# Performance work log

Hardware: AMD Instinct MI355X
Metric: run time of the kernel (lower is better)

The kernel has to match this reference:

```python
import jax, jax.numpy as jnp
import numpy as np
from math import sqrt

LOCAL_WINDOW = 32
STRIDE = 64


def _sparse_mask(L):
    # L_Q == L_K path of DozerAttention:
    #  - local window: diagonals at offsets 0..local_window//2 (both signs)
    #  - strided: diagonals at offsets 0, stride+1, 2*(stride+1), ... (both signs)
    i = jnp.arange(L)[:, None]
    j = jnp.arange(L)[None, :]
    d = jnp.abs(i - j)
    local = d <= (LOCAL_WINDOW // 2)
    strided = (d % (STRIDE + 1)) == 0
    return (local | strided).astype(jnp.float32)  # [L, L]


def setup_inputs() -> dict:
    key = jax.random.key(0)
    B, L, H, D = 2, 2048, 8, 64
    kq, kk, kv = jax.random.split(key, 3)
    queries = jax.random.normal(kq, (B, L, H, D), dtype=jnp.float32)
    keys = jax.random.normal(kk, (B, L, H, D), dtype=jnp.float32)
    values = jax.random.normal(kv, (B, L, H, D), dtype=jnp.float32)
    # TriangularCausalMask: True above the diagonal -> masked with -inf
    causal = jnp.triu(jnp.ones((L, L), dtype=bool), k=1)
    attn_mask = jnp.broadcast_to(causal[None, None], (B, 1, L, L))
    return {"queries": queries, "keys": keys, "values": values, "attn_mask": attn_mask}


def reference(queries, keys, values, attn_mask):
    B, L, H, D = queries.shape
    scale = 1.0 / sqrt(D)
    sm = _sparse_mask(L)  # [L, L]
    # Original fills a zero-initialized dense score tensor only at selected key
    # columns per query row; equivalent to dense QK^T elementwise-masked by sm
    # (non-selected entries stay exactly 0, NOT -inf -- faithful quirk).
    scores = jnp.einsum('blhe,bshe->bhls', queries, keys) * sm  # [B,H,L,L]
    scores = jnp.where(attn_mask, -jnp.inf, scores)
    A = jax.nn.softmax(scale * scores, axis=-1)  # dropout p=0.0 in this config
    V = jnp.einsum('bhls,bshd->blhd', A, values)  # [B,L,H,D]
    return V
```

## Files before the change

### kernel.cpp

```cpp
#include <hip/hip_runtime.h>
#include <hip/hip_bf16.h>

#define B_ 2
#define L_ 2048
#define H_ 8
#define D_ 64
#define SP_ 65
#define NC_ 128
#define RS_ 512

typedef __attribute__((ext_vector_type(8))) short bf16x8;
typedef __attribute__((ext_vector_type(16))) float f32x16;

static __device__ inline short f2bf(float x) {
    return __builtin_bit_cast(short, __float2bfloat16(x));
}

static __device__ inline bf16x8 ld8_bf16(const float* __restrict__ p) {
    float4 a = *(const float4*)p;
    float4 b = *(const float4*)(p + 4);
    bf16x8 r;
    r[0]=f2bf(a.x); r[1]=f2bf(a.y); r[2]=f2bf(a.z); r[3]=f2bf(a.w);
    r[4]=f2bf(b.x); r[5]=f2bf(b.y); r[6]=f2bf(b.z); r[7]=f2bf(b.w);
    return r;
}

static __device__ inline bf16x8 ones_frag() {
    bf16x8 r;
    short o = f2bf(1.f);
    #pragma unroll
    for (int t = 0; t < 8; ++t) r[t] = o;
    return r;
}

__global__ __launch_bounds__(256) void partials_k(const float* __restrict__ q,
                                                  const float* __restrict__ kk,
                                                  const float* __restrict__ v,
                                                  float* __restrict__ csum1,
                                                  float* __restrict__ pA,
                                                  float* __restrict__ zA,
                                                  float* __restrict__ pB,
                                                  float* __restrict__ zB) {
    __shared__ float LDS[4608];
    int wib  = threadIdx.x >> 6;
    int lane = threadIdx.x & 63;
    int half = lane >> 5, ln = lane & 31;
    int blk  = blockIdx.x;

    if (blk < 512) {
        int tb = wib >> 1;
        int hf = wib & 1;
        int team = blk * 2 + tb;
        int bh = team >> 6;
        int T  = (team & 63) << 5;
        int h = bh & 7, b = bh >> 3;
        const size_t base = (size_t)b * L_ * RS_ + (size_t)h * D_;
        float* Pw = LDS + tb * 2176;
        int d0 = 32 * hf;

        bf16x8 bv[4];
        #pragma unroll
        for (int kb = 0; kb < 4; ++kb) {
            #pragma unroll
            for (int jj = 0; jj < 8; ++jj) {
                int jr = T - 16 + kb * 16 + half * 8 + jj;
                jr = jr < 0 ? 0 : (jr > L_ - 1 ? L_ - 1 : jr);
                bv[kb][jj] = f2bf(v[base + (size_t)jr * RS_ + d0 + ln]);
            }
        }

        const float* qrow = q + base + (size_t)(T + ln) * RS_;
        bf16x8 aq[4];
        #pragma unroll
        for (int kb = 0; kb < 4; ++kb) aq[kb] = ld8_bf16(qrow + kb * 16 + half * 8);

        int j = T - 16 + 32 * hf + ln;
        j = j < 0 ? 0 : (j > L_ - 1 ? L_ - 1 : j);
        const float* krow = kk + base + (size_t)j * RS_;
        f32x16 acc = {};
        #pragma unroll
        for (int kb = 0; kb < 4; ++kb) {
            bf16x8 kf = ld8_bf16(krow + kb * 16 + half * 8);
            acc = __builtin_amdgcn_mfma_f32_32x32x16_bf16(aq[kb], kf, acc, 0, 0, 0);
        }

        #pragma unroll
        for (int r = 0; r < 16; ++r) {
            int m = (r & 3) + 8 * (r >> 2) + 4 * half;
            float w;
            if (hf == 0) {
                bool act = (ln >= m) && (ln <= m + 16) && (T - 16 + ln >= 0);
                w = act ? (__expf(0.125f * acc[r]) - 1.f) : 0.f;
                if ((m < 16) && (ln >= 16) && (ln <= m + 16)) w += 1.f;
            } else {
                bool act = (ln <= m - 16);
                w = act ? (__expf(0.125f * acc[r]) - 1.f) : 0.f;
                if ((m >= 16) && (ln <= m - 16)) w += 1.f;
            }
            Pw[m * 68 + d0 + ln] = w;
        }
        __syncthreads();

        f32x16 p = {}; f32x16 po = {};
        bf16x8 ones = ones_frag();
        #pragma unroll
        for (int kb = 0; kb < 4; ++kb) {
            int k0 = kb * 16 + half * 8;
            const float* pr = &Pw[ln * 68 + k0];
            float4 x = *(const float4*)pr;
            float4 y = *(const float4*)(pr + 4);
            bf16x8 ap;
            ap[0]=f2bf(x.x); ap[1]=f2bf(x.y); ap[2]=f2bf(x.z); ap[3]=f2bf(x.w);
            ap[4]=f2bf(y.x); ap[5]=f2bf(y.y); ap[6]=f2bf(y.z); ap[7]=f2bf(y.w);
            p = __builtin_amdgcn_mfma_f32_32x32x16_bf16(ap, bv[kb], p, 0, 0, 0);
            if (hf == 0)
                po = __builtin_amdgcn_mfma_f32_32x32x16_bf16(ap, ones, po, 0, 0, 0);
        }

        float* pAr = pA + (size_t)bh * L_ * D_;
        float* zAr = zA + (size_t)bh * L_;
        #pragma unroll
        for (int r = 0; r < 16; ++r) {
            int m = (r & 3) + 8 * (r >> 2) + 4 * half;
            int i = T + m;
            pAr[(size_t)i * D_ + d0 + ln] = p[r];
            if (hf == 0 && ln == 0)
                zAr[i] = po[r] - (float)((m & 15) + 1);
        }
    } else if (blk < 772) {
        int us = (blk - 512) * 4 + wib;
        int bh = us / SP_;
        int r  = us % SP_;
        int h = bh & 7, b = bh >> 3;
        const size_t base = (size_t)b * L_ * RS_ + (size_t)h * D_;
        float* Pw = LDS + wib * 1152;

        bf16x8 bv0[2], bv1[2];
        #pragma unroll
        for (int kb = 0; kb < 2; ++kb) {
            int k0 = kb * 16 + half * 8;
            #pragma unroll
            for (int jj = 0; jj < 8; ++jj) {
                int lv = r + SP_ * (k0 + jj);
                lv = lv > L_ - 1 ? L_ - 1 : lv;
                const float* vr = v + base + (size_t)lv * RS_;
                bv0[kb][jj] = f2bf(vr[ln]);
                bv1[kb][jj] = f2bf(vr[32 + ln]);
            }
        }

        int lq = r + SP_ * ln;
        int lqc = lq > L_ - 1 ? L_ - 1 : lq;
        const float* qrow = q  + base + (size_t)lqc * RS_;
        const float* krow = kk + base + (size_t)lqc * RS_;
        f32x16 acc = {};
        #pragma unroll
        for (int kb = 0; kb < 4; ++kb) {
            bf16x8 a  = ld8_bf16(qrow + kb * 16 + half * 8);
            bf16x8 bb = ld8_bf16(krow + kb * 16 + half * 8);
            acc = __builtin_amdgcn_mfma_f32_32x32x16_bf16(a, bb, acc, 0, 0, 0);
        }
        #pragma unroll
        for (int rg = 0; rg < 16; ++rg) {
            int m = (rg & 3) + 8 * (rg >> 2) + 4 * half;
            bool act = (ln < m) && (r + SP_ * m < L_);
            Pw[m * 36 + ln] = act ? (__expf(0.125f * acc[rg]) - 1.f) : 0.f;
        }
        __syncthreads();

        f32x16 p0 = {}; f32x16 p1 = {}; f32x16 po = {};
        bf16x8 ones = ones_frag();
        #pragma unroll
        for (int kb = 0; kb < 2; ++kb) {
            int k0 = kb * 16 + half * 8;
            const float* pr = &Pw[ln * 36 + k0];
            float4 x = *(const float4*)pr;
            float4 y = *(const float4*)(pr + 4);
            bf16x8 ap;
            ap[0]=f2bf(x.x); ap[1]=f2bf(x.y); ap[2]=f2bf(x.z); ap[3]=f2bf(x.w);
            ap[4]=f2bf(y.x); ap[5]=f2bf(y.y); ap[6]=f2bf(y.z); ap[7]=f2bf(y.w);
            p0 = __builtin_amdgcn_mfma_f32_32x32x16_bf16(ap, bv0[kb], p0, 0, 0, 0);
            p1 = __builtin_amdgcn_mfma_f32_32x32x16_bf16(ap, bv1[kb], p1, 0, 0, 0);
            po = __builtin_amdgcn_mfma_f32_32x32x16_bf16(ap, ones,    po, 0, 0, 0);
        }
        float* pBr = pB + (size_t)bh * L_ * D_;
        float* zBr = zB + (size_t)bh * L_;
        #pragma unroll
        for (int rg = 0; rg < 16; ++rg) {
            int m = (rg & 3) + 8 * (rg >> 2) + 4 * half;
            int l = r + SP_ * m;
            if (l < L_) {
                pBr[(size_t)l * D_ + ln]      = p0[rg];
                pBr[(size_t)l * D_ + 32 + ln] = p1[rg];
                if (ln == 0) zBr[l] = po[rg];
            }
        }
    } else {
        int uc = (blk - 772) * 4 + wib;
        int c = uc & (NC_ - 1);
        int bh = uc >> 7;
        int h = bh & 7, b = bh >> 3;
        const float* vb = v + (size_t)(b * L_ + c * 16) * RS_ + h * D_ + lane;
        float s = 0.f;
        #pragma unroll
        for (int l = 0; l < 16; ++l) s += vb[l * RS_];
        csum1[(size_t)uc * D_ + lane] = s;
    }
}

__global__ __launch_bounds__(256) void combine_k(const float* __restrict__ csum1,
                                                 const float* __restrict__ pA,
                                                 const float* __restrict__ zA,
                                                 const float* __restrict__ pB,
                                                 const float* __restrict__ zB,
                                                 float* __restrict__ out) {
    int wib  = threadIdx.x >> 6;
    int lane = threadIdx.x & 63;
    int u = blockIdx.x * 4 + wib;
    int bh = u >> 8;
    int g  = u & 255;
    int i0 = g << 3;
    int c1 = i0 >> 4;
    int h = bh & 7, b = bh >> 3;

    const float* cs1 = csum1 + (size_t)bh * NC_ * D_ + lane;
    float s0 = 0.f, s1 = 0.f, s2 = 0.f, s3 = 0.f;
    int cc = 0;
    for (; cc + 4 <= c1; cc += 4) {
        s0 += cs1[(cc + 0) * D_]; s1 += cs1[(cc + 1) * D_];
        s2 += cs1[(cc + 2) * D_]; s3 += cs1[(cc + 3) * D_];
    }
    for (; cc < c1; ++cc) s0 += cs1[cc * D_];
    float pr = (s0 + s1) + (s2 + s3);

    const float* pAr = pA + (size_t)bh * L_ * D_;
    const float* pBr = pB + (size_t)bh * L_ * D_;
    const float* zAr = zA + (size_t)bh * L_;
    const float* zBr = zB + (size_t)bh * L_;
    const size_t obase = (size_t)b * L_ * RS_ + (size_t)h * D_;

    #pragma unroll
    for (int r = 0; r < 8; ++r) {
        int i = i0 + r;
        float num = pAr[(size_t)i * D_ + lane] + pBr[(size_t)i * D_ + lane] + pr;
        float inv = 1.f / (zAr[i] + zBr[i] + (float)(i + 1));
        out[obase + (size_t)i * RS_ + lane] = num * inv;
    }
}

extern "C" void kernel_launch(void* const* d_in, const int* in_sizes, int n_in,
                              void* d_out, int out_size, void* d_ws, size_t ws_size,
                              hipStream_t stream) {
    const float* q = (const float*)d_in[0];
    const float* k = (const float*)d_in[1];
    const float* v = (const float*)d_in[2];
    float* out = (float*)d_out;

    float* csum1 = (float*)d_ws;
    float* pA    = csum1 + (size_t)B_ * H_ * NC_ * D_;
    float* zA    = pA    + (size_t)B_ * H_ * L_ * D_;
    float* pB    = zA    + (size_t)B_ * H_ * L_;
    float* zB    = pB    + (size_t)B_ * H_ * L_ * D_;

    partials_k<<<1284, 256, 0, stream>>>(q, k, v, csum1, pA, zA, pB, zB);
    combine_k<<<1024, 256, 0, stream>>>(csum1, pA, zA, pB, zB, out);
}
```

Baseline: 112.0 us.

## Fuse local-window attention into the combine kernel to drop pA/zA round trip

Moves the local-window QK/softmax-weight/PV computation out of the partials kernel and into the final combine kernel, so its partial numerator and normalizer stay in registers and LDS instead of being written to and reread from global workspace. The first kernel now handles only the strided partials and the chunk column sums. This removes the pA/zA global traffic and the separate combine pass. In exchange, the second kernel becomes heavier with fewer blocks, and the two phases rebalance across the launches.

```diff
diff --git a/kernel.cpp b/kernel.cpp
--- a/kernel.cpp
+++ b/kernel.cpp
@@ -33,102 +33,20 @@
     return r;
 }
 
-__global__ __launch_bounds__(256) void partials_k(const float* __restrict__ q,
-                                                  const float* __restrict__ kk,
-                                                  const float* __restrict__ v,
-                                                  float* __restrict__ csum1,
-                                                  float* __restrict__ pA,
-                                                  float* __restrict__ zA,
-                                                  float* __restrict__ pB,
-                                                  float* __restrict__ zB) {
+__global__ __launch_bounds__(256) void stride_csum_k(const float* __restrict__ q,
+                                                     const float* __restrict__ kk,
+                                                     const float* __restrict__ v,
+                                                     float* __restrict__ csum1,
+                                                     float* __restrict__ pB,
+                                                     float* __restrict__ zB) {
     __shared__ float LDS[4608];
     int wib  = threadIdx.x >> 6;
     int lane = threadIdx.x & 63;
     int half = lane >> 5, ln = lane & 31;
     int blk  = blockIdx.x;
 
-    if (blk < 512) {
-        int tb = wib >> 1;
-        int hf = wib & 1;
-        int team = blk * 2 + tb;
-        int bh = team >> 6;
-        int T  = (team & 63) << 5;
-        int h = bh & 7, b = bh >> 3;
-        const size_t base = (size_t)b * L_ * RS_ + (size_t)h * D_;
-        float* Pw = LDS + tb * 2176;
-        int d0 = 32 * hf;
-
-        bf16x8 bv[4];
-        #pragma unroll
-        for (int kb = 0; kb < 4; ++kb) {
-            #pragma unroll
-            for (int jj = 0; jj < 8; ++jj) {
-                int jr = T - 16 + kb * 16 + half * 8 + jj;
-                jr = jr < 0 ? 0 : (jr > L_ - 1 ? L_ - 1 : jr);
-                bv[kb][jj] = f2bf(v[base + (size_t)jr * RS_ + d0 + ln]);
-            }
-        }
-
-        const float* qrow = q + base + (size_t)(T + ln) * RS_;
-        bf16x8 aq[4];
-        #pragma unroll
-        for (int kb = 0; kb < 4; ++kb) aq[kb] = ld8_bf16(qrow + kb * 16 + half * 8);
-
-        int j = T - 16 + 32 * hf + ln;
-        j = j < 0 ? 0 : (j > L_ - 1 ? L_ - 1 : j);
-        const float* krow = kk + base + (size_t)j * RS_;
-        f32x16 acc = {};
-        #pragma unroll
-        for (int kb = 0; kb < 4; ++kb) {
-            bf16x8 kf = ld8_bf16(krow + kb * 16 + half * 8);
-            acc = __builtin_amdgcn_mfma_f32_32x32x16_bf16(aq[kb], kf, acc, 0, 0, 0);
-        }
-
-        #pragma unroll
-        for (int r = 0; r < 16; ++r) {
-            int m = (r & 3) + 8 * (r >> 2) + 4 * half;
-            float w;
-            if (hf == 0) {
-                bool act = (ln >= m) && (ln <= m + 16) && (T - 16 + ln >= 0);
-                w = act ? (__expf(0.125f * acc[r]) - 1.f) : 0.f;
-                if ((m < 16) && (ln >= 16) && (ln <= m + 16)) w += 1.f;
-            } else {
-                bool act = (ln <= m - 16);
-                w = act ? (__expf(0.125f * acc[r]) - 1.f) : 0.f;
-                if ((m >= 16) && (ln <= m - 16)) w += 1.f;
-            }
-            Pw[m * 68 + d0 + ln] = w;
-        }
-        __syncthreads();
-
-        f32x16 p = {}; f32x16 po = {};
-        bf16x8 ones = ones_frag();
-        #pragma unroll
-        for (int kb = 0; kb < 4; ++kb) {
-            int k0 = kb * 16 + half * 8;
-            const float* pr = &Pw[ln * 68 + k0];
-            float4 x = *(const float4*)pr;
-            float4 y = *(const float4*)(pr + 4);
-            bf16x8 ap;
-            ap[0]=f2bf(x.x); ap[1]=f2bf(x.y); ap[2]=f2bf(x.z); ap[3]=f2bf(x.w);
-            ap[4]=f2bf(y.x); ap[5]=f2bf(y.y); ap[6]=f2bf(y.z); ap[7]=f2bf(y.w);
-            p = __builtin_amdgcn_mfma_f32_32x32x16_bf16(ap, bv[kb], p, 0, 0, 0);
-            if (hf == 0)
-                po = __builtin_amdgcn_mfma_f32_32x32x16_bf16(ap, ones, po, 0, 0, 0);
-        }
-
-        float* pAr = pA + (size_t)bh * L_ * D_;
-        float* zAr = zA + (size_t)bh * L_;
-        #pragma unroll
-        for (int r = 0; r < 16; ++r) {
-            int m = (r & 3) + 8 * (r >> 2) + 4 * half;
-            int i = T + m;
-            pAr[(size_t)i * D_ + d0 + ln] = p[r];
-            if (hf == 0 && ln == 0)
-                zAr[i] = po[r] - (float)((m & 15) + 1);
-        }
-    } else if (blk < 772) {
-        int us = (blk - 512) * 4 + wib;
+    if (blk < 260) {
+        int us = blk * 4 + wib;
         int bh = us / SP_;
         int r  = us % SP_;
         int h = bh & 7, b = bh >> 3;
@@ -196,7 +114,7 @@
             }
         }
     } else {
-        int uc = (blk - 772) * 4 + wib;
+        int uc = (blk - 260) * 4 + wib;
         int c = uc & (NC_ - 1);
         int bh = uc >> 7;
         int h = bh & 7, b = bh >> 3;
@@ -208,43 +126,117 @@
     }
 }
 
-__global__ __launch_bounds__(256) void combine_k(const float* __restrict__ csum1,
-                                                 const float* __restrict__ pA,
-                                                 const float* __restrict__ zA,
-                                                 const float* __restrict__ pB,
-                                                 const float* __restrict__ zB,
-                                                 float* __restrict__ out) {
+__global__ __launch_bounds__(256) void local_final_k(const float* __restrict__ q,
+                                                     const float* __restrict__ kk,
+                                                     const float* __restrict__ v,
+                                                     const float* __restrict__ csum1,
+                                                     const float* __restrict__ pB,
+                                                     const float* __restrict__ zB,
+                                                     float* __restrict__ out) {
+    __shared__ float Pws[2][32 * 68];
+    __shared__ float zs[2][32];
     int wib  = threadIdx.x >> 6;
     int lane = threadIdx.x & 63;
-    int u = blockIdx.x * 4 + wib;
-    int bh = u >> 8;
-    int g  = u & 255;
-    int i0 = g << 3;
-    int c1 = i0 >> 4;
+    int half = lane >> 5, ln = lane & 31;
+    int tb = wib >> 1;
+    int hf = wib & 1;
+    int team = blockIdx.x * 2 + tb;
+    int bh = team >> 6;
+    int T  = (team & 63) << 5;
     int h = bh & 7, b = bh >> 3;
-
-    const float* cs1 = csum1 + (size_t)bh * NC_ * D_ + lane;
+    const size_t base = (size_t)b * L_ * RS_ + (size_t)h * D_;
+    float* Pw = Pws[tb];
+    int d0 = 32 * hf;
+
+    bf16x8 bv[4];
+    #pragma unroll
+    for (int kb = 0; kb < 4; ++kb) {
+        #pragma unroll
+        for (int jj = 0; jj < 8; ++jj) {
+            int jr = T - 16 + kb * 16 + half * 8 + jj;
+            jr = jr < 0 ? 0 : (jr > L_ - 1 ? L_ - 1 : jr);
+            bv[kb][jj] = f2bf(v[base + (size_t)jr * RS_ + d0 + ln]);
+        }
+    }
+
+    const float* qrow = q + base + (size_t)(T + ln) * RS_;
+    bf16x8 aq[4];
+    #pragma unroll
+    for (int kb = 0; kb < 4; ++kb) aq[kb] = ld8_bf16(qrow + kb * 16 + half * 8);
+
+    int j = T - 16 + d0 + ln;
+    j = j < 0 ? 0 : (j > L_ - 1 ? L_ - 1 : j);
+    const float* krow = kk + base + (size_t)j * RS_;
+    f32x16 acc = {};
+    #pragma unroll
+    for (int kb = 0; kb < 4; ++kb) {
+        bf16x8 kf = ld8_bf16(krow + kb * 16 + half * 8);
+        acc = __builtin_amdgcn_mfma_f32_32x32x16_bf16(aq[kb], kf, acc, 0, 0, 0);
+    }
+
+    #pragma unroll
+    for (int r = 0; r < 16; ++r) {
+        int m = (r & 3) + 8 * (r >> 2) + 4 * half;
+        float w;
+        if (hf == 0) {
+            bool act = (ln >= m) && (ln <= m + 16) && (T - 16 + ln >= 0);
+            w = act ? (__expf(0.125f * acc[r]) - 1.f) : 0.f;
+            if ((m < 16) && (ln >= 16) && (ln <= m + 16)) w += 1.f;
+        } else {
+            bool act = (ln <= m - 16);
+            w = act ? (__expf(0.125f * acc[r]) - 1.f) : 0.f;
+            if ((m >= 16) && (ln <= m - 16)) w += 1.f;
+        }
+        Pw[m * 68 + d0 + ln] = w;
+    }
+    __syncthreads();
+
+    f32x16 p = {}; f32x16 po = {};
+    bf16x8 ones = ones_frag();
+    #pragma unroll
+    for (int kb = 0; kb < 4; ++kb) {
+        int k0 = kb * 16 + half * 8;
+        const float* pr = &Pw[ln * 68 + k0];
+        float4 x = *(const float4*)pr;
+        float4 y = *(const float4*)(pr + 4);
+        bf16x8 ap;
+        ap[0]=f2bf(x.x); ap[1]=f2bf(x.y); ap[2]=f2bf(x.z); ap[3]=f2bf(x.w);
+        ap[4]=f2bf(y.x); ap[5]=f2bf(y.y); ap[6]=f2bf(y.z); ap[7]=f2bf(y.w);
+        p = __builtin_amdgcn_mfma_f32_32x32x16_bf16(ap, bv[kb], p, 0, 0, 0);
+        if (hf == 0)
+            po = __builtin_amdgcn_mfma_f32_32x32x16_bf16(ap, ones, po, 0, 0, 0);
+    }
+    if (hf == 0 && ln == 0) {
+        #pragma unroll
+        for (int r = 0; r < 16; ++r) {
+            int m = (r & 3) + 8 * (r >> 2) + 4 * half;
+            zs[tb][m] = po[r];
+        }
+    }
+
+    int c1b = T >> 4;
+    const float* cs1 = csum1 + (size_t)bh * NC_ * D_ + d0 + ln;
     float s0 = 0.f, s1 = 0.f, s2 = 0.f, s3 = 0.f;
     int cc = 0;
-    for (; cc + 4 <= c1; cc += 4) {
+    for (; cc + 4 <= c1b; cc += 4) {
         s0 += cs1[(cc + 0) * D_]; s1 += cs1[(cc + 1) * D_];
         s2 += cs1[(cc + 2) * D_]; s3 += cs1[(cc + 3) * D_];
     }
-    for (; cc < c1; ++cc) s0 += cs1[cc * D_];
+    for (; cc < c1b; ++cc) s0 += cs1[cc * D_];
     float pr = (s0 + s1) + (s2 + s3);
-
-    const float* pAr = pA + (size_t)bh * L_ * D_;
+    float ch = cs1[c1b * D_];
+    __syncthreads();
+
     const float* pBr = pB + (size_t)bh * L_ * D_;
-    const float* zAr = zA + (size_t)bh * L_;
     const float* zBr = zB + (size_t)bh * L_;
-    const size_t obase = (size_t)b * L_ * RS_ + (size_t)h * D_;
-
-    #pragma unroll
-    for (int r = 0; r < 8; ++r) {
-        int i = i0 + r;
-        float num = pAr[(size_t)i * D_ + lane] + pBr[(size_t)i * D_ + lane] + pr;
-        float inv = 1.f / (zAr[i] + zBr[i] + (float)(i + 1));
-        out[obase + (size_t)i * RS_ + lane] = num * inv;
+    #pragma unroll
+    for (int r = 0; r < 16; ++r) {
+        int m = (r & 3) + 8 * (r >> 2) + 4 * half;
+        int i = T + m;
+        float num = p[r] + pr + ((m & 16) ? ch : 0.f) + pBr[(size_t)i * D_ + d0 + ln];
+        float zloc = zs[tb][m] - (float)((m & 15) + 1);
+        float inv = 1.f / (zloc + zBr[i] + (float)(i + 1));
+        out[base + (size_t)i * RS_ + d0 + ln] = num * inv;
     }
 }
 
@@ -257,11 +249,9 @@
     float* out = (float*)d_out;
 
     float* csum1 = (float*)d_ws;
-    float* pA    = csum1 + (size_t)B_ * H_ * NC_ * D_;
-    float* zA    = pA    + (size_t)B_ * H_ * L_ * D_;
-    float* pB    = zA    + (size_t)B_ * H_ * L_;
+    float* pB    = csum1 + (size_t)B_ * H_ * NC_ * D_;
     float* zB    = pB    + (size_t)B_ * H_ * L_ * D_;
 
-    partials_k<<<1284, 256, 0, stream>>>(q, k, v, csum1, pA, zA, pB, zB);
-    combine_k<<<1024, 256, 0, stream>>>(csum1, pA, zA, pB, zB, out);
-}
+    stride_csum_k<<<772, 256, 0, stream>>>(q, k, v, csum1, pB, zB);
+    local_final_k<<<512, 256, 0, stream>>>(q, k, v, csum1, pB, zB, out);
+}
```

Measured after the change: 114.2 us. No clear change (+1.9%).
